# Kernel tuning notes

Measured on AMD Instinct MI355X. Metric: run time of the kernel, lower is better.

## Reference

```python
import jax, jax.numpy as jnp
import numpy as np

LN_EPS = 1e-5

def _layernorm(h, gamma, beta):
    mu = jnp.mean(h, axis=-1, keepdims=True)
    var = jnp.mean(jnp.square(h - mu), axis=-1, keepdims=True)
    return (h - mu) * jax.lax.rsqrt(var + LN_EPS) * gamma + beta

def setup_inputs() -> dict:
    key = jax.random.key(0)
    ks = jax.random.split(key, 8)
    B, T, D, H = 64, 512, 512, 1024
    x = jax.random.normal(ks[0], (B, T, D), dtype=jnp.float32)
    s_in = 1.0 / np.sqrt(D)
    s_h = 1.0 / np.sqrt(H)
    W_in = jax.random.uniform(ks[1], (H, D), minval=-s_in, maxval=s_in, dtype=jnp.float32)
    b_in = jax.random.uniform(ks[2], (H,), minval=-s_in, maxval=s_in, dtype=jnp.float32)
    W_state = jax.random.uniform(ks[3], (H, H), minval=-s_h, maxval=s_h, dtype=jnp.float32)
    b_state = jax.random.uniform(ks[4], (H,), minval=-s_h, maxval=s_h, dtype=jnp.float32)
    decay = jnp.zeros((H,), dtype=jnp.float32)  # nn.Parameter(torch.zeros(hidden))
    ln_gamma = jnp.ones((H,), dtype=jnp.float32)
    ln_beta = jnp.zeros((H,), dtype=jnp.float32)
    return {"x": x, "W_in": W_in, "b_in": b_in, "W_state": W_state,
            "b_state": b_state, "decay": decay, "ln_gamma": ln_gamma, "ln_beta": ln_beta}

def reference(x, W_in, b_in, W_state, b_state, decay, ln_gamma, ln_beta):
    B, T, D = x.shape
    H = W_in.shape[0]
    d = jax.nn.sigmoid(decay)  # [H]
    # Precompute the input drive for all steps: [B,T,H] -> time-major [T,B,H]
    u = jnp.einsum('btd,hd->bth', x, W_in) + b_in
    u = jnp.swapaxes(u, 0, 1)

    def step(state, u_t):
        driven = jnp.tanh(u_t + state @ W_state.T + b_state)
        state = d * state + (1.0 - d) * driven
        y = _layernorm(state, ln_gamma, ln_beta)
        return state, y

    init = jnp.zeros((B, H), dtype=x.dtype)
    _, ys = jax.lax.scan(step, init, u)  # ys: [T,B,H]
    return jnp.swapaxes(ys, 0, 1)  # [B,T,H]
```

## Files before the change

kernel.cpp:

```cpp
#include <hip/hip_runtime.h>
#include <hip/hip_bf16.h>


#define B_    64
#define T_    512
#define H_    1024
#define GCOLS 64

typedef __attribute__((ext_vector_type(8))) __bf16 bf16x8;
typedef __attribute__((ext_vector_type(4))) float f32x4;
typedef __attribute__((ext_vector_type(4))) unsigned uint32x4;

static __device__ __forceinline__ unsigned f2bf_bits(float f) {
    unsigned u = __float_as_uint(f);
    return (u + 0x7FFFu + ((u >> 16) & 1u)) >> 16;
}

static __device__ __forceinline__ float fast_tanh(float x) {
    x = fminf(fmaxf(x, -15.f), 15.f);
    const float e = __expf(2.f * x);
    return 1.f - 2.f * __builtin_amdgcn_rcpf(e + 1.f);
}

#define SLOADC(dst, base, BOFF)                                               \
    asm volatile("global_load_dwordx4 %0, %1, off offset:%2 sc0 sc1"          \
                 : "=&v"(dst) : "v"(base), "n"(BOFF))
#define ULOAD(dst, base)                                                      \
    asm volatile("global_load_dword %0, %1, off"                              \
                 : "=&v"(dst) : "v"(base))

#define BM 128
#define BN 128
#define BKK 32
#define LDT 40

__global__ __launch_bounds__(256)
void u_gemm(const float* __restrict__ X, const float* __restrict__ Win,
            const float* __restrict__ bin, float* __restrict__ U) {
    __shared__ unsigned short Al[BM][LDT];
    __shared__ unsigned short Bl[BN][LDT];
    const int tid = threadIdx.x;
    const int m0 = blockIdx.y * BM;
    const int n0 = blockIdx.x * BN;
    const int l  = tid & 63;
    const int w  = tid >> 6;
    const int wr = (w >> 1) * 64, wc = (w & 1) * 64;
    const int fr = l & 15, fk = (l >> 4) * 8;

    f32x4 acc[4][4];
#pragma unroll
    for (int m = 0; m < 4; ++m)
#pragma unroll
        for (int n = 0; n < 4; ++n) acc[m][n] = f32x4{0.f, 0.f, 0.f, 0.f};

    const int sr = tid >> 1;
    const int sc = (tid & 1) * 16;

    for (int k0 = 0; k0 < 512; k0 += BKK) {
        const float* ap = X   + (size_t)(m0 + sr) * 512 + k0 + sc;
        const float* bp = Win + (size_t)(n0 + sr) * 512 + k0 + sc;
        float a[16], b[16];
#pragma unroll
        for (int j = 0; j < 4; ++j) {
            *(float4*)&a[j * 4] = *(const float4*)(ap + j * 4);
            *(float4*)&b[j * 4] = *(const float4*)(bp + j * 4);
        }
        __syncthreads();
#pragma unroll
        for (int j = 0; j < 16; ++j) {
            Al[sr][sc + j] = (unsigned short)f2bf_bits(a[j]);
            Bl[sr][sc + j] = (unsigned short)f2bf_bits(b[j]);
        }
        __syncthreads();

        bf16x8 af[4], bf[4];
#pragma unroll
        for (int m = 0; m < 4; ++m)
            af[m] = *(const bf16x8*)&Al[wr + m * 16 + fr][fk];
#pragma unroll
        for (int n = 0; n < 4; ++n)
            bf[n] = *(const bf16x8*)&Bl[wc + n * 16 + fr][fk];
#pragma unroll
        for (int m = 0; m < 4; ++m)
#pragma unroll
            for (int n = 0; n < 4; ++n)
                acc[m][n] = __builtin_amdgcn_mfma_f32_16x16x32_bf16(
                    af[m], bf[n], acc[m][n], 0, 0, 0);
    }

#pragma unroll
    for (int m = 0; m < 4; ++m) {
#pragma unroll
        for (int n = 0; n < 4; ++n) {
            const int col = n0 + wc + n * 16 + fr;
            const float bb = bin[col];
#pragma unroll
            for (int r = 0; r < 4; ++r) {
                const int row = m0 + wr + m * 16 + (l >> 4) * 4 + r;
                U[(size_t)row * 1024 + col] = acc[m][n][r] + bb;
            }
        }
    }
}

__global__ __launch_bounds__(256, 1)
void rec_tag3(const float* __restrict__ Wst, float* __restrict__ UY,
              const float* __restrict__ b_state, const float* __restrict__ decay,
              const float* __restrict__ gamma, const float* __restrict__ beta,
              unsigned* __restrict__ Sbuf) {
    extern __shared__ __align__(16) unsigned char smem[];
    unsigned short* Wl = (unsigned short*)smem;
    unsigned*       Sl = (unsigned*)(smem + 131072);
    float*          muS = (float*)(smem + 131072);
    float*          rsS = muS + 16;

    const int tid  = threadIdx.x;
    const int bid  = blockIdx.x;
    const int rg   = bid >> 4;
    const int cbk  = bid & 15;
    const int h0   = cbk * GCOLS;
    const int wave = tid >> 6;
    const int lane = tid & 63;
    const int c    = lane & 15;
    const int rgrp = lane >> 4;
    const int mycol = h0 + wave * 16 + c;
    const int lrow  = wave * 4 + rgrp;

    {
        const int col = tid >> 2;
        const int sub = tid & 3;
        const float* wr_ = Wst + (size_t)(h0 + col) * H_ + sub * 256;
#pragma unroll
        for (int i = 0; i < 32; ++i) {
            float4 f0 = *(const float4*)(wr_ + i * 8);
            float4 f1 = *(const float4*)(wr_ + i * 8 + 4);
            unsigned short* dst = Wl + ((size_t)(sub * 32 + i) * 64 + col) * 8;
            dst[0] = (unsigned short)f2bf_bits(f0.x);
            dst[1] = (unsigned short)f2bf_bits(f0.y);
            dst[2] = (unsigned short)f2bf_bits(f0.z);
            dst[3] = (unsigned short)f2bf_bits(f0.w);
            dst[4] = (unsigned short)f2bf_bits(f1.x);
            dst[5] = (unsigned short)f2bf_bits(f1.y);
            dst[6] = (unsigned short)f2bf_bits(f1.z);
            dst[7] = (unsigned short)f2bf_bits(f1.w);
        }
    }

    const float d_c  = 1.f / (1.f + __expf(-decay[mycol]));
    const float od_c = 1.f - d_c;
    const float bs_c = b_state[mycol];
    const float g_c  = gamma[mycol];
    const float be_c = beta[mycol];

    float sold[4] = {0.f, 0.f, 0.f, 0.f};
    int brow[4];
#pragma unroll
    for (int r = 0; r < 4; ++r) brow[r] = rg * 16 + rgrp * 4 + r;

    float yv[4] = {0.f, 0.f, 0.f, 0.f};
    float uun[4], uu[4];
#pragma unroll
    for (int r = 0; r < 4; ++r)
        uun[r] = UY[(size_t)brow[r] * T_ * H_ + mycol];

    unsigned* const Sg = Sbuf + ((size_t)rg * 3 << 14);
    const int swzW = (lrow & 7) << 2;
    const int swzR = (c & 7) << 2;

    uint32x4 tw[16];
    {
        const unsigned* lb0 = Sg + (size_t)lrow * 1024 + c * 4;
#pragma unroll
        for (int j = 0; j < 16; ++j) SLOADC(tw[j], lb0, j * 256);
        asm volatile("s_waitcnt vmcnt(0)" ::: "memory");
        __builtin_amdgcn_sched_barrier(0);
    }

    __syncthreads();

    for (int t = 0; t < T_; ++t) {
        const unsigned* Sr = Sg + ((size_t)(t % 3) << 14);
        unsigned*       Sw = Sg + ((size_t)((t + 1) % 3) << 14);
        const unsigned tagr = (unsigned)t, tagw = (unsigned)(t + 1);
        const unsigned* lb = Sr + (size_t)lrow * 1024 + c * 4;

        __syncthreads();

        asm volatile("s_waitcnt vmcnt(4)" ::: "memory");
        __builtin_amdgcn_sched_barrier(0);
#pragma unroll
        for (int r = 0; r < 4; ++r) uu[r] = uun[r];

        {
            int spin = 0;
            for (;;) {
                unsigned mn = 0xFFFFFFFFu;
#pragma unroll
                for (int j = 0; j < 16; ++j) {
                    unsigned m01 = tw[j][0] < tw[j][1] ? tw[j][0] : tw[j][1];
                    unsigned m23 = tw[j][2] < tw[j][3] ? tw[j][2] : tw[j][3];
                    unsigned m = m01 < m23 ? m01 : m23;
                    mn = mn < m ? mn : m;
                }
                if (__all((mn >> 16) == tagr)) break;
                if (((++spin) & 7) == 7)
                    __builtin_amdgcn_fence(__ATOMIC_ACQUIRE, "agent");
                __builtin_amdgcn_s_sleep(1);
#pragma unroll
                for (int j = 0; j < 16; ++j) SLOADC(tw[j], lb, j * 256);
                asm volatile("s_waitcnt vmcnt(0)" ::: "memory");
                __builtin_amdgcn_sched_barrier(0);
            }
        }

        float s1 = 0.f, s2 = 0.f;
#pragma unroll
        for (int j = 0; j < 16; ++j) {
#pragma unroll
            for (int k = 0; k < 4; ++k) {
                const float v = __uint_as_float(tw[j][k] << 16);
                s1 += v;
                s2 = fmaf(v, v, s2);
            }
        }
        s1 += __shfl_xor(s1, 1); s2 += __shfl_xor(s2, 1);
        s1 += __shfl_xor(s1, 2); s2 += __shfl_xor(s2, 2);
        s1 += __shfl_xor(s1, 4); s2 += __shfl_xor(s2, 4);
        s1 += __shfl_xor(s1, 8); s2 += __shfl_xor(s2, 8);
        const float mu_l = s1 * (1.f / (float)H_);
        const float rs_l = rsqrtf(s2 * (1.f / (float)H_) - mu_l * mu_l + 1e-5f);

#pragma unroll
        for (int j = 0; j < 16; ++j) {
            const unsigned p0 = __builtin_amdgcn_perm(tw[j][1], tw[j][0], 0x05040100u);
            const unsigned p1 = __builtin_amdgcn_perm(tw[j][3], tw[j][2], 0x05040100u);
            const int idx = (j * 32 + c * 2) ^ swzW;
            *(uint2*)&Sl[lrow * 512 + idx] = uint2{p0, p1};
        }
        __syncthreads();

        f32x4 a0 = {0.f, 0.f, 0.f, 0.f}, a1 = a0, a2 = a0, a3 = a0;
#pragma unroll
        for (int kk = 0; kk < 32; kk += 4) {
#pragma unroll
            for (int q = 0; q < 4; ++q) {
                const int ai = ((kk + q) * 16 + rgrp * 4) ^ swzR;
                const uint32x4 aw = *(const uint32x4*)&Sl[c * 512 + ai];
                const bf16x8 af = __builtin_bit_cast(bf16x8, aw);
                const bf16x8 bf = *(const bf16x8*)(Wl +
                    ((size_t)((kk + q) * 4 + rgrp) * 64 + wave * 16 + c) * 8);
                if (q == 0) a0 = __builtin_amdgcn_mfma_f32_16x16x32_bf16(af, bf, a0, 0, 0, 0);
                if (q == 1) a1 = __builtin_amdgcn_mfma_f32_16x16x32_bf16(af, bf, a1, 0, 0, 0);
                if (q == 2) a2 = __builtin_amdgcn_mfma_f32_16x16x32_bf16(af, bf, a2, 0, 0, 0);
                if (q == 3) a3 = __builtin_amdgcn_mfma_f32_16x16x32_bf16(af, bf, a3, 0, 0, 0);
            }
        }
        const f32x4 acc = (a0 + a1) + (a2 + a3);

        float sprev[4];
#pragma unroll
        for (int r = 0; r < 4; ++r) {
            sprev[r] = sold[r];
            const float pre = acc[r] + uu[r] + bs_c;
            const float sn  = d_c * sold[r] + od_c * fast_tanh(pre);
            sold[r] = sn;
            __hip_atomic_store(&Sw[(size_t)(rgrp * 4 + r) * 1024 + mycol],
                               (tagw << 16) | f2bf_bits(sn),
                               __ATOMIC_RELAXED, __HIP_MEMORY_SCOPE_AGENT);
        }

        if (t + 1 < T_) {
#pragma unroll
            for (int r = 0; r < 4; ++r) {
                const float* ub = UY + ((size_t)brow[r] * T_ + (t + 1)) * H_ + mycol;
                ULOAD(uun[r], ub);
            }
            const unsigned* lbn =
                Sg + ((size_t)((t + 1) % 3) << 14) + (size_t)lrow * 1024 + c * 4;
#pragma unroll
            for (int j = 0; j < 16; ++j) SLOADC(tw[j], lbn, j * 256);
        }

        __syncthreads();
        if (c == 0) { muS[lrow] = mu_l; rsS[lrow] = rs_l; }
        __syncthreads();
        if (t >= 2) {
#pragma unroll
            for (int r = 0; r < 4; ++r)
                UY[((size_t)brow[r] * T_ + (t - 2)) * H_ + mycol] = yv[r];
        }
        if (t > 0) {
#pragma unroll
            for (int r = 0; r < 4; ++r) {
                const int R = rgrp * 4 + r;
                yv[r] = (sprev[r] - muS[R]) * rsS[R] * g_c + be_c;
            }
        }
    }

    {
#pragma unroll
        for (int r = 0; r < 4; ++r)
            UY[((size_t)brow[r] * T_ + (T_ - 2)) * H_ + mycol] = yv[r];

        const unsigned* Sr = Sg + ((size_t)(T_ % 3) << 14);
        const unsigned tagr = (unsigned)T_;
        const unsigned* lb = Sr + (size_t)lrow * 1024 + c * 4;
        int spin = 0;
#pragma unroll
        for (int j = 0; j < 16; ++j) SLOADC(tw[j], lb, j * 256);
        for (;;) {
            asm volatile("s_waitcnt vmcnt(0)" ::: "memory");
            __builtin_amdgcn_sched_barrier(0);
            unsigned mn = 0xFFFFFFFFu;
#pragma unroll
            for (int j = 0; j < 16; ++j) {
                unsigned m01 = tw[j][0] < tw[j][1] ? tw[j][0] : tw[j][1];
                unsigned m23 = tw[j][2] < tw[j][3] ? tw[j][2] : tw[j][3];
                unsigned m = m01 < m23 ? m01 : m23;
                mn = mn < m ? mn : m;
            }
            if (__all((mn >> 16) == tagr)) break;
            if (((++spin) & 7) == 7)
                __builtin_amdgcn_fence(__ATOMIC_ACQUIRE, "agent");
            __builtin_amdgcn_s_sleep(1);
#pragma unroll
            for (int j = 0; j < 16; ++j) SLOADC(tw[j], lb, j * 256);
        }
        float s1 = 0.f, s2 = 0.f;
#pragma unroll
        for (int j = 0; j < 16; ++j) {
#pragma unroll
            for (int k = 0; k < 4; ++k) {
                const float v = __uint_as_float(tw[j][k] << 16);
                s1 += v;
                s2 = fmaf(v, v, s2);
            }
        }
        s1 += __shfl_xor(s1, 1); s2 += __shfl_xor(s2, 1);
        s1 += __shfl_xor(s1, 2); s2 += __shfl_xor(s2, 2);
        s1 += __shfl_xor(s1, 4); s2 += __shfl_xor(s2, 4);
        s1 += __shfl_xor(s1, 8); s2 += __shfl_xor(s2, 8);
        const float mu_l = s1 * (1.f / (float)H_);
        const float rs_l = rsqrtf(s2 * (1.f / (float)H_) - mu_l * mu_l + 1e-5f);
        __syncthreads();
        if (c == 0) { muS[lrow] = mu_l; rsS[lrow] = rs_l; }
        __syncthreads();
#pragma unroll
        for (int r = 0; r < 4; ++r) {
            const int R = rgrp * 4 + r;
            UY[((size_t)brow[r] * T_ + (T_ - 1)) * H_ + mycol] =
                (sold[r] - muS[R]) * rsS[R] * g_c + be_c;
        }
    }
}

extern "C" void kernel_launch(void* const* d_in, const int* in_sizes, int n_in,
                              void* d_out, int out_size, void* d_ws, size_t ws_size,
                              hipStream_t stream) {
    const float* x   = (const float*)d_in[0];
    const float* Win = (const float*)d_in[1];
    const float* bin = (const float*)d_in[2];
    const float* Wst = (const float*)d_in[3];
    const float* bst = (const float*)d_in[4];
    const float* dec = (const float*)d_in[5];
    const float* lng = (const float*)d_in[6];
    const float* lnb = (const float*)d_in[7];
    float* out = (float*)d_out;

    unsigned char* ws = (unsigned char*)d_ws;
    unsigned* Sbuf = (unsigned*)(ws + 4096);

    hipFuncSetAttribute(reinterpret_cast<const void*>(rec_tag3),
                        hipFuncAttributeMaxDynamicSharedMemorySize, 163840);

    hipMemsetAsync(Sbuf, 0, 4u * 3u * 16u * 1024u * 4u, stream);
    u_gemm<<<dim3(8, 256), 256, 0, stream>>>(x, Win, bin, out);
    rec_tag3<<<64, 256, 163840, stream>>>(Wst, out, bst, dec, lng, lnb, Sbuf);
}
```

Baseline: 1.656 ms.

## Double-issue state polling loads and fix vmcnt accounting in recurrent kernel

The recurrent kernel now issues two speculative loads of the next step's tagged state (twA right after the state write, twB after the layernorm stats), so the tag check usually succeeds on the first or second copy without entering a spin loop. Stores go through inline asm with dummy stores to a scratch buffer in the early steps, which keeps the vmcnt count fixed so a constant s_waitcnt vmcnt(20) can be used. Several __syncthreads are replaced by raw s_barrier plus an explicit lgkmcnt wait. This lowers the cross-block handoff latency per timestep, at the cost of extra global traffic and more register pressure from the second 16x uint4 buffer.

```diff
diff --git a/kernel.cpp b/kernel.cpp
--- a/kernel.cpp
+++ b/kernel.cpp
@@ -28,6 +28,16 @@
 #define ULOAD(dst, base)                                                      \
     asm volatile("global_load_dword %0, %1, off"                              \
                  : "=&v"(dst) : "v"(base))
+#define PSTORE(base, data)                                                    \
+    asm volatile("global_store_dword %0, %1, off sc0 sc1"                     \
+                 :: "v"(base), "v"(data))
+#define YSTORE(base, data)                                                    \
+    asm volatile("global_store_dword %0, %1, off" :: "v"(base), "v"(data))
+#define VMCNT20() asm volatile("s_waitcnt vmcnt(20)" ::: "memory")
+#define VMCNT0()  asm volatile("s_waitcnt vmcnt(0)" ::: "memory")
+#define LGKM0()   asm volatile("s_waitcnt lgkmcnt(0)" ::: "memory")
+#define SBAR()    __builtin_amdgcn_s_barrier()
+#define SCHEDB()  __builtin_amdgcn_sched_barrier(0)
 
 #define BM 128
 #define BN 128
@@ -104,10 +114,10 @@
 }
 
 __global__ __launch_bounds__(256, 1)
-void rec_tag3(const float* __restrict__ Wst, float* __restrict__ UY,
+void rec_tag4(const float* __restrict__ Wst, float* __restrict__ UY,
               const float* __restrict__ b_state, const float* __restrict__ decay,
               const float* __restrict__ gamma, const float* __restrict__ beta,
-              unsigned* __restrict__ Sbuf) {
+              unsigned* __restrict__ Sbuf, unsigned* __restrict__ ydump) {
     extern __shared__ __align__(16) unsigned char smem[];
     unsigned short* Wl = (unsigned short*)smem;
     unsigned*       Sl = (unsigned*)(smem + 131072);
@@ -158,58 +168,84 @@
     for (int r = 0; r < 4; ++r) brow[r] = rg * 16 + rgrp * 4 + r;
 
     float yv[4] = {0.f, 0.f, 0.f, 0.f};
-    float uun[4], uu[4];
-#pragma unroll
-    for (int r = 0; r < 4; ++r)
-        uun[r] = UY[(size_t)brow[r] * T_ * H_ + mycol];
-
     unsigned* const Sg = Sbuf + ((size_t)rg * 3 << 14);
     const int swzW = (lrow & 7) << 2;
     const int swzR = (c & 7) << 2;
-
-    uint32x4 tw[16];
+    unsigned* const yd = ydump + (bid << 8) + tid;
+
+    __syncthreads();
+
+    uint32x4 twA[16], twB[16];
+    float uun[4], uu[4];
     {
+#pragma unroll
+        for (int r = 0; r < 4; ++r) {
+            const float* ub = UY + (size_t)brow[r] * T_ * H_ + mycol;
+            ULOAD(uun[r], ub);
+        }
         const unsigned* lb0 = Sg + (size_t)lrow * 1024 + c * 4;
 #pragma unroll
-        for (int j = 0; j < 16; ++j) SLOADC(tw[j], lb0, j * 256);
-        asm volatile("s_waitcnt vmcnt(0)" ::: "memory");
-        __builtin_amdgcn_sched_barrier(0);
-    }
-
-    __syncthreads();
+        for (int j = 0; j < 16; ++j) SLOADC(twA[j], lb0, j * 256);
+#pragma unroll
+        for (int r = 0; r < 4; ++r) YSTORE(yd, 0u);
+#pragma unroll
+        for (int j = 0; j < 16; ++j) SLOADC(twB[j], lb0, j * 256);
+    }
 
     for (int t = 0; t < T_; ++t) {
-        const unsigned* Sr = Sg + ((size_t)(t % 3) << 14);
         unsigned*       Sw = Sg + ((size_t)((t + 1) % 3) << 14);
         const unsigned tagr = (unsigned)t, tagw = (unsigned)(t + 1);
-        const unsigned* lb = Sr + (size_t)lrow * 1024 + c * 4;
-
-        __syncthreads();
-
-        asm volatile("s_waitcnt vmcnt(4)" ::: "memory");
-        __builtin_amdgcn_sched_barrier(0);
+        const unsigned* lb =
+            Sg + ((size_t)(t % 3) << 14) + (size_t)lrow * 1024 + c * 4;
+
+        SBAR();
+        VMCNT20(); SCHEDB();
 #pragma unroll
         for (int r = 0; r < 4; ++r) uu[r] = uun[r];
 
         {
-            int spin = 0;
-            for (;;) {
-                unsigned mn = 0xFFFFFFFFu;
+            unsigned mn = 0xFFFFFFFFu;
+#pragma unroll
+            for (int j = 0; j < 16; ++j) {
+                unsigned m01 = twA[j][0] < twA[j][1] ? twA[j][0] : twA[j][1];
+                unsigned m23 = twA[j][2] < twA[j][3] ? twA[j][2] : twA[j][3];
+                unsigned m = m01 < m23 ? m01 : m23;
+                mn = mn < m ? mn : m;
+            }
+            if (!__all((mn >> 16) == tagr)) {
+                VMCNT0(); SCHEDB();
+                unsigned mb = 0xFFFFFFFFu;
 #pragma unroll
                 for (int j = 0; j < 16; ++j) {
-                    unsigned m01 = tw[j][0] < tw[j][1] ? tw[j][0] : tw[j][1];
-                    unsigned m23 = tw[j][2] < tw[j][3] ? tw[j][2] : tw[j][3];
+                    unsigned m01 = twB[j][0] < twB[j][1] ? twB[j][0] : twB[j][1];
+                    unsigned m23 = twB[j][2] < twB[j][3] ? twB[j][2] : twB[j][3];
                     unsigned m = m01 < m23 ? m01 : m23;
-                    mn = mn < m ? mn : m;
+                    mb = mb < m ? mb : m;
                 }
-                if (__all((mn >> 16) == tagr)) break;
-                if (((++spin) & 7) == 7)
-                    __builtin_amdgcn_fence(__ATOMIC_ACQUIRE, "agent");
-                __builtin_amdgcn_s_sleep(1);
-#pragma unroll
-                for (int j = 0; j < 16; ++j) SLOADC(tw[j], lb, j * 256);
-                asm volatile("s_waitcnt vmcnt(0)" ::: "memory");
-                __builtin_amdgcn_sched_barrier(0);
+                if (__all((mb >> 16) == tagr)) {
+#pragma unroll
+                    for (int j = 0; j < 16; ++j) twA[j] = twB[j];
+                } else {
+                    int spin = 0;
+                    for (;;) {
+                        if ((spin & 7) == 7)
+                            __builtin_amdgcn_fence(__ATOMIC_ACQUIRE, "agent");
+                        ++spin;
+                        __builtin_amdgcn_s_sleep(1);
+#pragma unroll
+                        for (int j = 0; j < 16; ++j) SLOADC(twA[j], lb, j * 256);
+                        VMCNT0(); SCHEDB();
+                        unsigned m2 = 0xFFFFFFFFu;
+#pragma unroll
+                        for (int j = 0; j < 16; ++j) {
+                            unsigned m01 = twA[j][0] < twA[j][1] ? twA[j][0] : twA[j][1];
+                            unsigned m23 = twA[j][2] < twA[j][3] ? twA[j][2] : twA[j][3];
+                            unsigned m = m01 < m23 ? m01 : m23;
+                            m2 = m2 < m ? m2 : m;
+                        }
+                        if (__all((m2 >> 16) == tagr)) break;
+                    }
+                }
             }
         }
 
@@ -218,7 +254,7 @@
         for (int j = 0; j < 16; ++j) {
 #pragma unroll
             for (int k = 0; k < 4; ++k) {
-                const float v = __uint_as_float(tw[j][k] << 16);
+                const float v = __uint_as_float(twA[j][k] << 16);
                 s1 += v;
                 s2 = fmaf(v, v, s2);
             }
@@ -232,12 +268,12 @@
 
 #pragma unroll
         for (int j = 0; j < 16; ++j) {
-            const unsigned p0 = __builtin_amdgcn_perm(tw[j][1], tw[j][0], 0x05040100u);
-            const unsigned p1 = __builtin_amdgcn_perm(tw[j][3], tw[j][2], 0x05040100u);
+            const unsigned p0 = __builtin_amdgcn_perm(twA[j][1], twA[j][0], 0x05040100u);
+            const unsigned p1 = __builtin_amdgcn_perm(twA[j][3], twA[j][2], 0x05040100u);
             const int idx = (j * 32 + c * 2) ^ swzW;
             *(uint2*)&Sl[lrow * 512 + idx] = uint2{p0, p1};
         }
-        __syncthreads();
+        LGKM0(); SBAR();
 
         f32x4 a0 = {0.f, 0.f, 0.f, 0.f}, a1 = a0, a2 = a0, a3 = a0;
 #pragma unroll
@@ -264,75 +300,103 @@
             const float pre = acc[r] + uu[r] + bs_c;
             const float sn  = d_c * sold[r] + od_c * fast_tanh(pre);
             sold[r] = sn;
-            __hip_atomic_store(&Sw[(size_t)(rgrp * 4 + r) * 1024 + mycol],
-                               (tagw << 16) | f2bf_bits(sn),
-                               __ATOMIC_RELAXED, __HIP_MEMORY_SCOPE_AGENT);
-        }
-
-        if (t + 1 < T_) {
+            unsigned* pa = &Sw[(size_t)(rgrp * 4 + r) * 1024 + mycol];
+            const unsigned pd = (tagw << 16) | f2bf_bits(sn);
+            PSTORE(pa, pd);
+        }
+        {
+            const int tn = (t + 1 < T_) ? (t + 1) : (T_ - 1);
 #pragma unroll
             for (int r = 0; r < 4; ++r) {
-                const float* ub = UY + ((size_t)brow[r] * T_ + (t + 1)) * H_ + mycol;
+                const float* ub = UY + ((size_t)brow[r] * T_ + tn) * H_ + mycol;
                 ULOAD(uun[r], ub);
             }
-            const unsigned* lbn =
-                Sg + ((size_t)((t + 1) % 3) << 14) + (size_t)lrow * 1024 + c * 4;
-#pragma unroll
-            for (int j = 0; j < 16; ++j) SLOADC(tw[j], lbn, j * 256);
-        }
-
-        __syncthreads();
+        }
+        const unsigned* lbn =
+            Sg + ((size_t)((t + 1) % 3) << 14) + (size_t)lrow * 1024 + c * 4;
+#pragma unroll
+        for (int j = 0; j < 16; ++j) SLOADC(twA[j], lbn, j * 256);
+        if (t >= 2) {
+#pragma unroll
+            for (int r = 0; r < 4; ++r) {
+                float* yt = UY + ((size_t)brow[r] * T_ + (t - 2)) * H_ + mycol;
+                YSTORE(yt, __float_as_uint(yv[r]));
+            }
+        } else {
+#pragma unroll
+            for (int r = 0; r < 4; ++r) YSTORE(yd, 0u);
+        }
+
+        SBAR();
         if (c == 0) { muS[lrow] = mu_l; rsS[lrow] = rs_l; }
-        __syncthreads();
-        if (t >= 2) {
-#pragma unroll
-            for (int r = 0; r < 4; ++r)
-                UY[((size_t)brow[r] * T_ + (t - 2)) * H_ + mycol] = yv[r];
-        }
-        if (t > 0) {
-#pragma unroll
-            for (int r = 0; r < 4; ++r) {
-                const int R = rgrp * 4 + r;
-                yv[r] = (sprev[r] - muS[R]) * rsS[R] * g_c + be_c;
-            }
-        }
+        LGKM0(); SBAR();
+#pragma unroll
+        for (int r = 0; r < 4; ++r) {
+            const int R = rgrp * 4 + r;
+            yv[r] = (sprev[r] - muS[R]) * rsS[R] * g_c + be_c;
+        }
+#pragma unroll
+        for (int j = 0; j < 16; ++j) SLOADC(twB[j], lbn, j * 256);
     }
 
     {
-#pragma unroll
-        for (int r = 0; r < 4; ++r)
-            UY[((size_t)brow[r] * T_ + (T_ - 2)) * H_ + mycol] = yv[r];
-
-        const unsigned* Sr = Sg + ((size_t)(T_ % 3) << 14);
+        VMCNT0(); SCHEDB();
+#pragma unroll
+        for (int r = 0; r < 4; ++r) {
+            float* yt = UY + ((size_t)brow[r] * T_ + (T_ - 2)) * H_ + mycol;
+            YSTORE(yt, __float_as_uint(yv[r]));
+        }
         const unsigned tagr = (unsigned)T_;
-        const unsigned* lb = Sr + (size_t)lrow * 1024 + c * 4;
-        int spin = 0;
-#pragma unroll
-        for (int j = 0; j < 16; ++j) SLOADC(tw[j], lb, j * 256);
-        for (;;) {
-            asm volatile("s_waitcnt vmcnt(0)" ::: "memory");
-            __builtin_amdgcn_sched_barrier(0);
-            unsigned mn = 0xFFFFFFFFu;
+        const unsigned* lb =
+            Sg + ((size_t)(T_ % 3) << 14) + (size_t)lrow * 1024 + c * 4;
+        unsigned mn = 0xFFFFFFFFu;
+#pragma unroll
+        for (int j = 0; j < 16; ++j) {
+            unsigned m01 = twA[j][0] < twA[j][1] ? twA[j][0] : twA[j][1];
+            unsigned m23 = twA[j][2] < twA[j][3] ? twA[j][2] : twA[j][3];
+            unsigned m = m01 < m23 ? m01 : m23;
+            mn = mn < m ? mn : m;
+        }
+        if (!__all((mn >> 16) == tagr)) {
+            unsigned mb = 0xFFFFFFFFu;
 #pragma unroll
             for (int j = 0; j < 16; ++j) {
-                unsigned m01 = tw[j][0] < tw[j][1] ? tw[j][0] : tw[j][1];
-                unsigned m23 = tw[j][2] < tw[j][3] ? tw[j][2] : tw[j][3];
+                unsigned m01 = twB[j][0] < twB[j][1] ? twB[j][0] : twB[j][1];
+                unsigned m23 = twB[j][2] < twB[j][3] ? twB[j][2] : twB[j][3];
                 unsigned m = m01 < m23 ? m01 : m23;
-                mn = mn < m ? mn : m;
-            }
-            if (__all((mn >> 16) == tagr)) break;
-            if (((++spin) & 7) == 7)
-                __builtin_amdgcn_fence(__ATOMIC_ACQUIRE, "agent");
-            __builtin_amdgcn_s_sleep(1);
-#pragma unroll
-            for (int j = 0; j < 16; ++j) SLOADC(tw[j], lb, j * 256);
+                mb = mb < m ? mb : m;
+            }
+            if (__all((mb >> 16) == tagr)) {
+#pragma unroll
+                for (int j = 0; j < 16; ++j) twA[j] = twB[j];
+            } else {
+                int spin = 0;
+                for (;;) {
+                    if ((spin & 7) == 7)
+                        __builtin_amdgcn_fence(__ATOMIC_ACQUIRE, "agent");
+                    ++spin;
+                    __builtin_amdgcn_s_sleep(1);
+#pragma unroll
+                    for (int j = 0; j < 16; ++j) SLOADC(twA[j], lb, j * 256);
+                    VMCNT0(); SCHEDB();
+                    unsigned m2 = 0xFFFFFFFFu;
+#pragma unroll
+                    for (int j = 0; j < 16; ++j) {
+                        unsigned m01 = twA[j][0] < twA[j][1] ? twA[j][0] : twA[j][1];
+                        unsigned m23 = twA[j][2] < twA[j][3] ? twA[j][2] : twA[j][3];
+                        unsigned m = m01 < m23 ? m01 : m23;
+                        m2 = m2 < m ? m2 : m;
+                    }
+                    if (__all((m2 >> 16) == tagr)) break;
+                }
+            }
         }
         float s1 = 0.f, s2 = 0.f;
 #pragma unroll
         for (int j = 0; j < 16; ++j) {
 #pragma unroll
             for (int k = 0; k < 4; ++k) {
-                const float v = __uint_as_float(tw[j][k] << 16);
+                const float v = __uint_as_float(twA[j][k] << 16);
                 s1 += v;
                 s2 = fmaf(v, v, s2);
             }
@@ -369,12 +433,14 @@
     float* out = (float*)d_out;
 
     unsigned char* ws = (unsigned char*)d_ws;
-    unsigned* Sbuf = (unsigned*)(ws + 4096);
-
-    hipFuncSetAttribute(reinterpret_cast<const void*>(rec_tag3),
+    unsigned* Sbuf  = (unsigned*)(ws + 4096);
+    unsigned* ydump = (unsigned*)(ws + 4096 + 786432);
+
+    hipFuncSetAttribute(reinterpret_cast<const void*>(rec_tag4),
                         hipFuncAttributeMaxDynamicSharedMemorySize, 163840);
 
     hipMemsetAsync(Sbuf, 0, 4u * 3u * 16u * 1024u * 4u, stream);
     u_gemm<<<dim3(8, 256), 256, 0, stream>>>(x, Win, bin, out);
-    rec_tag3<<<64, 256, 163840, stream>>>(Wst, out, bst, dec, lng, lnb, Sbuf);
+    rec_tag4<<<64, 256, 163840, stream>>>(Wst, out, bst, dec, lng, lnb,
+                                          Sbuf, ydump);
 }
```

Measured after the change: 2.009 ms. 21.3% more time.
